# Kernel optimization log

Hardware: AMD Instinct MI355X
Metric: run time of the kernel (lower is better)

Reference implementation:

```python
import jax, jax.numpy as jnp
import numpy as np
import math

G = 512        # graphs in batch
N_PER = 256    # nodes per graph (regular batching)
H = 128        # hidden_size == rnn_hidden_size
DEG = 8        # avg degree
RATIO = 0.8    # TopKPooling ratio
N = G * N_PER
E = N * DEG
N_HIDDEN = 3   # n_hidden_layers


def setup_inputs() -> dict:
    key = jax.random.key(0)
    ks = jax.random.split(key, 20)
    x = jax.random.normal(ks[0], (N, H), jnp.float32)
    m = N_PER * DEG
    src_l = jax.random.randint(ks[1], (G, m), 0, N_PER)
    dst_l = jax.random.randint(ks[2], (G, m), 0, N_PER)
    off = (jnp.arange(G, dtype=jnp.int32) * N_PER)[:, None]
    edge_index = jnp.stack([(src_l + off).reshape(-1), (dst_l + off).reshape(-1)]).astype(jnp.int32)
    s = 1.0 / math.sqrt(H)
    def w(k, shape):
        return jax.random.normal(k, shape, jnp.float32) * s
    return {
        'x': x, 'edge_index': edge_index,
        'W0': w(ks[3], (H, H)), 'b0': jnp.zeros((H,), jnp.float32), 'p0': w(ks[4], (H,)),
        'W1': w(ks[5], (H, H)), 'b1': jnp.zeros((H,), jnp.float32), 'p1': w(ks[6], (H,)),
        'W2': w(ks[7], (H, H)), 'b2': jnp.zeros((H,), jnp.float32), 'p2': w(ks[8], (H,)),
        'Wg': w(ks[9], (H, 1)), 'bg': jnp.zeros((1,), jnp.float32),
    }


def _gcn(x, src, dst, w_e, W, b, n_nodes):
    # GCNConv with self loops: out = D^-1/2 (A+I) D^-1/2 (x W) + b, masked edges have w_e=0
    h = x @ W
    deg = jax.ops.segment_sum(w_e, dst, num_segments=n_nodes) + 1.0  # +1 self loop
    dinv = jax.lax.rsqrt(deg)
    norm = w_e * dinv[src] * dinv[dst]
    agg = jax.ops.segment_sum(h[src] * norm[:, None], dst, num_segments=n_nodes)
    agg = agg + h * (dinv * dinv)[:, None]   # self-loop term
    return agg + b


def _topk(x, src, dst, w_e, p, n_per):
    # TopKPooling: score = x.p/||p||, keep top ceil(ratio*n) per graph, scale by tanh(score)
    k = math.ceil(RATIO * n_per)
    score = (x @ p) / jnp.linalg.norm(p)
    _, idx = jax.lax.top_k(score.reshape(G, n_per), k)           # [G,k] local idx
    perm = (idx + (jnp.arange(G, dtype=idx.dtype) * n_per)[:, None]).reshape(-1)
    x_new = x[perm] * jnp.tanh(score[perm])[:, None]
    nmap = jnp.full((G * n_per,), -1, jnp.int32).at[perm].set(jnp.arange(G * k, dtype=jnp.int32))
    ms, md = nmap[src], nmap[dst]
    valid = (ms >= 0) & (md >= 0)
    src2 = jnp.where(valid, ms, 0)
    dst2 = jnp.where(valid, md, 0)
    return x_new, src2, dst2, w_e * valid.astype(w_e.dtype), k


def _attpool(x, n_per, Wg, bg):
    # GlobalAttention: softmax(gate) over nodes of each graph, weighted sum
    gate = (x @ Wg + bg).reshape(G, n_per)
    a = jax.nn.softmax(gate, axis=1)
    return jnp.einsum('gn,gnh->gh', a, x.reshape(G, n_per, H))


def reference(x, edge_index, W0, b0, p0, W1, b1, p1, W2, b2, p2, Wg, bg):
    src, dst = edge_index[0], edge_index[1]
    w_e = jnp.ones((E,), jnp.float32)
    n_per = N_PER
    h = jax.nn.relu(_gcn(x, src, dst, w_e, W0, b0, G * n_per))
    h, src, dst, w_e, n_per = _topk(h, src, dst, w_e, p0, n_per)
    out = _attpool(h, n_per, Wg, bg)
    for (W, b, p) in ((W1, b1, p1), (W2, b2, p2)):  # n_hidden_layers - 1 = 2
        h = jax.nn.relu(_gcn(h, src, dst, w_e, W, b, G * n_per))
        h, src, dst, w_e, n_per = _topk(h, src, dst, w_e, p, n_per)
        out = out + _attpool(h, n_per, Wg, bg)
    return out
```

## Files before the change

### kernel.cpp

```cpp
#include <hip/hip_runtime.h>
#include <math.h>

#define GCOUNT 512
#define HDIM 128
#define EPG 2048
#define E_TOTAL (GCOUNT * EPG)
#define DEADE 0xFFFFFFFFu

typedef __attribute__((ext_vector_type(8))) short short8;
typedef __attribute__((ext_vector_type(4))) float f32x4;

__device__ inline unsigned short f2bf(float f) {
  unsigned int u = __float_as_uint(f);
  return (unsigned short)((u + 0x7FFFu + ((u >> 16) & 1u)) >> 16);
}
__device__ inline float bf2f(unsigned short s) {
  return __uint_as_float(((unsigned int)s) << 16);
}

__global__ __launch_bounds__(256) void k_wsplit(const float* __restrict__ W,
                                                unsigned short* __restrict__ out) {
  int t = blockIdx.x * 256 + threadIdx.x;
  int lane = t & 63;
  int ct = (t >> 6) & 7;
  int kc = t >> 9;
  int kbase = kc * 32 + (lane >> 4) * 8;
  int col = ct * 16 + (lane & 15);
#pragma unroll
  for (int j = 0; j < 8; j++) {
    float w = W[(size_t)(kbase + j) * HDIM + col];
    unsigned short h0 = f2bf(w);  float g0 = bf2f(h0);
    float r1 = w - g0;
    unsigned short h1 = f2bf(r1); float g1 = bf2f(h1);
    unsigned short h2 = f2bf(r1 - g1);
    int base = (kc * 8 + ct) * 512 + lane * 8 + j;
    out[base]         = h0;
    out[base + 16384] = h1;
    out[base + 32768] = h2;
  }
}

__global__ __launch_bounds__(1024, 1) void k_net(
    const float* __restrict__ xIn, const int* __restrict__ ei0,
    const unsigned short* __restrict__ Ws0,
    const unsigned short* __restrict__ Ws1,
    const unsigned short* __restrict__ Ws2,
    const float* __restrict__ b0, const float* __restrict__ p0,
    const float* __restrict__ b1, const float* __restrict__ p1,
    const float* __restrict__ b2, const float* __restrict__ p2,
    const float* __restrict__ Wg, const float* __restrict__ bgp,
    float* __restrict__ outp) {

  __shared__ __align__(16) float h_s[256 * 132];
  __shared__ unsigned int es[EPG];
  __shared__ unsigned short ss[EPG];
  __shared__ __align__(16) int deg[256];
  __shared__ int cnt[256];
  __shared__ int ofs[256];
  __shared__ int rp[260];
  __shared__ float dinv_s[256];
  __shared__ float rawsc_s[256];
  __shared__ float hd[256];
  __shared__ float sc[256];
  __shared__ int   idx[256];
  __shared__ float tn[256];
  __shared__ float accout[128];
  __shared__ float part[512];
  __shared__ float red[8];
  __shared__ float snorm_s;

  int g = blockIdx.x, t = threadIdx.x;
  int lane = t & 63, wv = t >> 6;
  int eb = g * EPG;
  float bgv = bgp[0];

  if (t < 256) deg[t] = 0;
  if (t < 128) accout[t] = 0.f;
  __syncthreads();
  {
    const float4* xg = (const float4*)(xIn + (size_t)g * 256 * HDIM);
    for (int i = t; i < 8192; i += 1024) {
      int r = i >> 5, q = i & 31;
      *(float4*)&h_s[r * 132 + (q << 2)] = xg[i];
    }
  }
#pragma unroll
  for (int q = 0; q < 2; q++) {
    int e = t + q * 1024;
    int s_ = ei0[eb + e] - g * 256;
    int d_ = ei0[E_TOTAL + eb + e] - g * 256;
    es[e] = (unsigned)s_ | ((unsigned)d_ << 16);
    atomicAdd(&deg[d_], 1);
  }
  __syncthreads();

  int n = 256;
#pragma unroll 1
  for (int layer = 0; layer < 3; layer++) {
    const unsigned short* Ws = (layer == 0) ? Ws0 : (layer == 1 ? Ws1 : Ws2);
    const float* bias = (layer == 0) ? b0 : (layer == 1 ? b1 : b2);
    const float* p    = (layer == 0) ? p0 : (layer == 1 ? p1 : p2);
    int k = (layer == 0) ? 205 : (layer == 1 ? 164 : 132);
    int T = (n + 15) >> 4;

    if (wv < T) {
      int rbase = wv * 16;
      int arow = lane & 15, kgrp = (lane >> 4) * 8;
      f32x4 acc[8];
#pragma unroll
      for (int ct = 0; ct < 8; ct++) acc[ct] = (f32x4){0.f, 0.f, 0.f, 0.f};
#pragma unroll
      for (int kc = 0; kc < 4; kc++) {
        short8 fa0, fa1, fa2;
        {
          const float* ap = &h_s[(rbase + arow) * 132 + kc * 32 + kgrp];
          float4 x0 = *(const float4*)ap;
          float4 x1 = *(const float4*)(ap + 4);
          float v[8] = {x0.x, x0.y, x0.z, x0.w, x1.x, x1.y, x1.z, x1.w};
#pragma unroll
          for (int j = 0; j < 8; j++) {
            float a = v[j];
            unsigned short q0 = f2bf(a);  float g0 = bf2f(q0);
            float r1 = a - g0;
            unsigned short q1 = f2bf(r1); float g1 = bf2f(q1);
            unsigned short q2 = f2bf(r1 - g1);
            fa0[j] = (short)q0; fa1[j] = (short)q1; fa2[j] = (short)q2;
          }
        }
#pragma unroll
        for (int ct = 0; ct < 8; ct++) {
          const unsigned short* wb = Ws + (kc * 8 + ct) * 512 + lane * 8;
          short8 w0 = *(const short8*)wb;
          short8 w1 = *(const short8*)(wb + 16384);
          short8 w2 = *(const short8*)(wb + 32768);
          acc[ct] = __builtin_amdgcn_mfma_f32_16x16x32_bf16(fa0, w0, acc[ct], 0, 0, 0);
          acc[ct] = __builtin_amdgcn_mfma_f32_16x16x32_bf16(fa0, w1, acc[ct], 0, 0, 0);
          acc[ct] = __builtin_amdgcn_mfma_f32_16x16x32_bf16(fa1, w0, acc[ct], 0, 0, 0);
          acc[ct] = __builtin_amdgcn_mfma_f32_16x16x32_bf16(fa1, w1, acc[ct], 0, 0, 0);
          acc[ct] = __builtin_amdgcn_mfma_f32_16x16x32_bf16(fa0, w2, acc[ct], 0, 0, 0);
          acc[ct] = __builtin_amdgcn_mfma_f32_16x16x32_bf16(fa2, w0, acc[ct], 0, 0, 0);
        }
      }
      int crow = (lane >> 4) * 4, ccol = lane & 15;
#pragma unroll
      for (int ct = 0; ct < 8; ct++)
#pragma unroll
        for (int reg = 0; reg < 4; reg++)
          h_s[(rbase + crow + reg) * 132 + ct * 16 + ccol] = acc[ct][reg];
    }
    __syncthreads();

    if (t < 256) dinv_s[t] = rsqrtf((float)deg[t] + 1.0f);
    if (wv == 0) {
      int4 c4 = *(const int4*)&deg[lane << 2];
      int s4 = c4.x + c4.y + c4.z + c4.w;
      int run = s4;
#pragma unroll
      for (int o = 1; o < 64; o <<= 1) {
        int v = __shfl_up(run, o);
        if (lane >= o) run += v;
      }
      int base = run - s4;
      int v1 = base + c4.x, v2 = v1 + c4.y, v3 = v2 + c4.z;
      int li = lane << 2;
      rp[li] = base; rp[li + 1] = v1; rp[li + 2] = v2; rp[li + 3] = v3;
      ofs[li] = base; ofs[li + 1] = v1; ofs[li + 2] = v2; ofs[li + 3] = v3;
      if (lane == 63) rp[256] = run;
    }
    if (wv == 1) {
      float q = p[lane] * p[lane] + p[lane + 64] * p[lane + 64];
#pragma unroll
      for (int o = 32; o > 0; o >>= 1) q += __shfl_xor(q, o);
      if (lane == 0) snorm_s = sqrtf(q);
    }
    if (t >= 128 && t < 512) {
      int i = t - 128;
      part[i] = (i < 128) ? bias[i] : (i < 256 ? p[i - 128] : Wg[i - 256]);
    }
    __syncthreads();

    if (t < 256) { cnt[t] = -1; deg[t] = 0; }
    for (int e = t; e < EPG; e += 1024) {
      unsigned u = es[e];
      if (u != DEADE) {
        int pos = atomicAdd(&ofs[u >> 16], 1);
        ss[pos] = (unsigned short)(u & 0xFFFFu);
      }
    }
    __syncthreads();

    {
      int dstT = t >> 2;
      int cq = (t & 3) << 3;
      bool dok = dstT < n;
      int begT = 0, endT = 0;
      float dvT = 0.f;
      if (dok) { begT = rp[dstT]; endT = rp[dstT + 1]; dvT = dinv_s[dstT]; }
      float sp = 0.f, sg = 0.f;
#pragma unroll 1
      for (int grp = 0; grp < 4; grp++) {
        int c0 = (grp << 5) + cq;
        float4 r0 = make_float4(0.f, 0.f, 0.f, 0.f);
        float4 r1 = make_float4(0.f, 0.f, 0.f, 0.f);
        if (dok) {
          float4 u0 = make_float4(0.f, 0.f, 0.f, 0.f);
          float4 u1 = make_float4(0.f, 0.f, 0.f, 0.f);
          int j = begT;
          for (; j + 2 <= endT; j += 2) {
            int sa = ss[j], sb = ss[j + 1];
            float wa = dinv_s[sa], wb2 = dinv_s[sb];
            const float* ha = &h_s[sa * 132 + c0];
            const float* hbp = &h_s[sb * 132 + c0];
            float4 xa0 = *(const float4*)ha;
            float4 xa1 = *(const float4*)(ha + 4);
            float4 xb0 = *(const float4*)hbp;
            float4 xb1 = *(const float4*)(hbp + 4);
            u0.x = fmaf(wa, xa0.x, u0.x); u0.y = fmaf(wa, xa0.y, u0.y);
            u0.z = fmaf(wa, xa0.z, u0.z); u0.w = fmaf(wa, xa0.w, u0.w);
            u1.x = fmaf(wa, xa1.x, u1.x); u1.y = fmaf(wa, xa1.y, u1.y);
            u1.z = fmaf(wa, xa1.z, u1.z); u1.w = fmaf(wa, xa1.w, u1.w);
            u0.x = fmaf(wb2, xb0.x, u0.x); u0.y = fmaf(wb2, xb0.y, u0.y);
            u0.z = fmaf(wb2, xb0.z, u0.z); u0.w = fmaf(wb2, xb0.w, u0.w);
            u1.x = fmaf(wb2, xb1.x, u1.x); u1.y = fmaf(wb2, xb1.y, u1.y);
            u1.z = fmaf(wb2, xb1.z, u1.z); u1.w = fmaf(wb2, xb1.w, u1.w);
          }
          if (j < endT) {
            int sa = ss[j];
            float wa = dinv_s[sa];
            const float* ha = &h_s[sa * 132 + c0];
            float4 xa0 = *(const float4*)ha;
            float4 xa1 = *(const float4*)(ha + 4);
            u0.x = fmaf(wa, xa0.x, u0.x); u0.y = fmaf(wa, xa0.y, u0.y);
            u0.z = fmaf(wa, xa0.z, u0.z); u0.w = fmaf(wa, xa0.w, u0.w);
            u1.x = fmaf(wa, xa1.x, u1.x); u1.y = fmaf(wa, xa1.y, u1.y);
            u1.z = fmaf(wa, xa1.z, u1.z); u1.w = fmaf(wa, xa1.w, u1.w);
          }
          const float* hdp = &h_s[dstT * 132 + c0];
          float4 s0 = *(const float4*)hdp;
          float4 s1 = *(const float4*)(hdp + 4);
          float4 bb0 = *(const float4*)&part[c0];
          float4 bb1 = *(const float4*)&part[c0 + 4];
          r0.x = fmaxf(fmaf(dvT, fmaf(s0.x, dvT, u0.x), bb0.x), 0.f);
          r0.y = fmaxf(fmaf(dvT, fmaf(s0.y, dvT, u0.y), bb0.y), 0.f);
          r0.z = fmaxf(fmaf(dvT, fmaf(s0.z, dvT, u0.z), bb0.z), 0.f);
          r0.w = fmaxf(fmaf(dvT, fmaf(s0.w, dvT, u0.w), bb0.w), 0.f);
          r1.x = fmaxf(fmaf(dvT, fmaf(s1.x, dvT, u1.x), bb1.x), 0.f);
          r1.y = fmaxf(fmaf(dvT, fmaf(s1.y, dvT, u1.y), bb1.y), 0.f);
          r1.z = fmaxf(fmaf(dvT, fmaf(s1.z, dvT, u1.z), bb1.z), 0.f);
          r1.w = fmaxf(fmaf(dvT, fmaf(s1.w, dvT, u1.w), bb1.w), 0.f);
          float4 pp0 = *(const float4*)&part[128 + c0];
          float4 pp1 = *(const float4*)&part[128 + c0 + 4];
          float4 gg0 = *(const float4*)&part[256 + c0];
          float4 gg1 = *(const float4*)&part[256 + c0 + 4];
          sp += r0.x * pp0.x + r0.y * pp0.y + r0.z * pp0.z + r0.w * pp0.w
              + r1.x * pp1.x + r1.y * pp1.y + r1.z * pp1.z + r1.w * pp1.w;
          sg += r0.x * gg0.x + r0.y * gg0.y + r0.z * gg0.z + r0.w * gg0.w
              + r1.x * gg1.x + r1.y * gg1.y + r1.z * gg1.z + r1.w * gg1.w;
        }
        __syncthreads();
        if (dok) {
          *(float4*)&h_s[dstT * 132 + c0] = r0;
          *(float4*)&h_s[dstT * 132 + c0 + 4] = r1;
        }
      }
      __syncthreads();
      sp += __shfl_xor(sp, 1); sp += __shfl_xor(sp, 2);
      sg += __shfl_xor(sg, 1); sg += __shfl_xor(sg, 2);
      if (dok && (t & 3) == 0) { rawsc_s[dstT] = sp; hd[dstT] = sg; }
    }
    __syncthreads();

    float key = -INFINITY;
    int id = t & 255;
    if (t < n) key = rawsc_s[t];
    for (int size = 2; size <= 256; size <<= 1) {
      for (int stride = size >> 1; stride > 0; stride >>= 1) {
        if (stride > 32) {
          if (t < 256) { sc[t] = key; idx[t] = id; }
          __syncthreads();
          float pk = 0.f; int pi = 0;
          if (t < 256) { pk = sc[t ^ stride]; pi = idx[t ^ stride]; }
          __syncthreads();
          if (t < 256) {
            bool want = ((t & size) == 0);
            bool lowr = ((t & stride) == 0);
            bool mineFirst = (key > pk) || (key == pk && id < pi);
            if (mineFirst != (want == lowr)) { key = pk; id = pi; }
          }
        } else {
          if (t < 256) {
            float pk = __shfl_xor(key, stride);
            int pi = __shfl_xor(id, stride);
            bool want = ((t & size) == 0);
            bool lowr = ((t & stride) == 0);
            bool mineFirst = (key > pk) || (key == pk && id < pi);
            if (mineFirst != (want == lowr)) { key = pk; id = pi; }
          }
        }
      }
    }
    if (t < 256) idx[t] = id;
    __syncthreads();

    float gate = -INFINITY;
    if (t < k) {
      float tnv = tanhf(key / snorm_s);
      tn[t] = tnv;
      cnt[id] = t;
      gate = fmaf(hd[id], tnv, bgv);
    }
    if (wv < 4) {
      float m = gate;
#pragma unroll
      for (int o = 32; o > 0; o >>= 1) m = fmaxf(m, __shfl_xor(m, o));
      if (lane == 0) red[wv] = m;
    }
    __syncthreads();

    float ex = 0.f;
    if (wv < 4) {
      float m = fmaxf(fmaxf(red[0], red[1]), fmaxf(red[2], red[3]));
      ex = (t < k) ? __expf(gate - m) : 0.f;
      float s = ex;
#pragma unroll
      for (int o = 32; o > 0; o >>= 1) s += __shfl_xor(s, o);
      if (lane == 0) red[4 + wv] = s;
    } else if (wv >= 8 && layer < 2) {
      int tt = t - 512;
#pragma unroll
      for (int q = 0; q < 4; q++) {
        int e = tt + q * 512;
        unsigned u = es[e];
        unsigned o = DEADE;
        if (u != DEADE) {
          int ns = cnt[u & 0xFFFFu], nd = cnt[u >> 16];
          if (ns >= 0 && nd >= 0) o = (unsigned)ns | ((unsigned)nd << 16);
        }
        es[e] = o;
        if (o != DEADE) atomicAdd(&deg[o >> 16], 1);
      }
    }
    __syncthreads();

    if (t < 256) {
      float inv = 1.f / (red[4] + red[5] + red[6] + red[7]);
      float a = (t < k) ? ex * inv : 0.f;
      sc[t] = (layer == 2) ? a * tn[t] : a;
    }
    __syncthreads();

    if (layer < 2) {
      {
        int rT = t >> 2;
        int cq4 = (t & 3) << 3;
        bool rok = rT < k;
        int src = 0;
        float tr = 0.f;
        if (rok) { src = idx[rT]; tr = tn[rT]; }
#pragma unroll 1
        for (int grp = 0; grp < 4; grp++) {
          int c0 = (grp << 5) + cq4;
          float4 v0 = make_float4(0.f, 0.f, 0.f, 0.f);
          float4 v1 = make_float4(0.f, 0.f, 0.f, 0.f);
          if (rok) {
            const float* hp = &h_s[src * 132 + c0];
            v0 = *(const float4*)hp;
            v1 = *(const float4*)(hp + 4);
            v0.x *= tr; v0.y *= tr; v0.z *= tr; v0.w *= tr;
            v1.x *= tr; v1.y *= tr; v1.z *= tr; v1.w *= tr;
          }
          __syncthreads();
          if (rok) {
            *(float4*)&h_s[rT * 132 + c0] = v0;
            *(float4*)&h_s[rT * 132 + c0 + 4] = v1;
          }
        }
      }
      __syncthreads();
      if (t < 512) {
        int grp = t >> 7, c2 = t & 127;
        float pp = 0.f;
        for (int r = grp; r < k; r += 4) pp = fmaf(sc[r], h_s[r * 132 + c2], pp);
        part[t] = pp;
      }
      __syncthreads();
      if (t < 128) accout[t] += part[t] + part[128 + t] + part[256 + t] + part[384 + t];
      __syncthreads();
    } else {
      if (t < 512) {
        int grp = t >> 7, c2 = t & 127;
        float pp = 0.f;
        for (int r = grp; r < k; r += 4) pp = fmaf(sc[r], h_s[idx[r] * 132 + c2], pp);
        part[t] = pp;
      }
      __syncthreads();
      if (t < 128)
        outp[(size_t)g * HDIM + t] =
            accout[t] + part[t] + part[128 + t] + part[256 + t] + part[384 + t];
    }
    n = k;
  }
}

extern "C" void kernel_launch(void* const* d_in, const int* in_sizes, int n_in,
                              void* d_out, int out_size, void* d_ws, size_t ws_size,
                              hipStream_t stream) {
  const float* x  = (const float*)d_in[0];
  const int*   ei = (const int*)d_in[1];
  const float* W0 = (const float*)d_in[2];
  const float* b0 = (const float*)d_in[3];
  const float* p0 = (const float*)d_in[4];
  const float* W1 = (const float*)d_in[5];
  const float* b1 = (const float*)d_in[6];
  const float* p1 = (const float*)d_in[7];
  const float* W2 = (const float*)d_in[8];
  const float* b2 = (const float*)d_in[9];
  const float* p2 = (const float*)d_in[10];
  const float* Wg = (const float*)d_in[11];
  const float* bg = (const float*)d_in[12];
  float* out = (float*)d_out;

  unsigned char* ws = (unsigned char*)d_ws;
  unsigned short* Wsp0 = (unsigned short*)(ws);
  unsigned short* Wsp1 = (unsigned short*)(ws + 98304ull);
  unsigned short* Wsp2 = (unsigned short*)(ws + 196608ull);

  k_wsplit<<<8, 256, 0, stream>>>(W0, Wsp0);
  k_wsplit<<<8, 256, 0, stream>>>(W1, Wsp1);
  k_wsplit<<<8, 256, 0, stream>>>(W2, Wsp2);
  k_net<<<GCOUNT, 1024, 0, stream>>>(x, ei, Wsp0, Wsp1, Wsp2,
                                     b0, p0, b1, p1, b2, p2, Wg, bg, out);
}
```

Measured before the change: 233.7 us.

## Use 2-term bf16 split GEMM, halve aggregation passes, double-buffer bitonic sort

The weight and activation splitting drops from three bf16 terms to two, cutting MFMAs per tile from 6 to 4 and removing the third weight load. The GCN aggregation and top-k gather now process two 64-column halves per thread instead of four 32-column groups, which halves the edge-list walks and the barriers. The bitonic sort's cross-wave stages ping-pong between two shared buffers, so each stage needs one barrier instead of two. The reduced split lowers GEMM precision, which could change top-k selections on near-ties.

```diff
diff --git a/kernel.cpp b/kernel.cpp
--- a/kernel.cpp
+++ b/kernel.cpp
@@ -16,6 +16,26 @@
 }
 __device__ inline float bf2f(unsigned short s) {
   return __uint_as_float(((unsigned int)s) << 16);
+}
+__device__ inline float4 z4() { return make_float4(0.f, 0.f, 0.f, 0.f); }
+__device__ inline float4 ld4(const float* p) { return *(const float4*)p; }
+__device__ inline void fma4(float4& u, float w, float4 x) {
+  u.x = fmaf(w, x.x, u.x); u.y = fmaf(w, x.y, u.y);
+  u.z = fmaf(w, x.z, u.z); u.w = fmaf(w, x.w, u.w);
+}
+__device__ inline float4 fin4(float4 u, float4 s, float4 b, float dv) {
+  float4 r;
+  r.x = fmaxf(fmaf(dv, fmaf(s.x, dv, u.x), b.x), 0.f);
+  r.y = fmaxf(fmaf(dv, fmaf(s.y, dv, u.y), b.y), 0.f);
+  r.z = fmaxf(fmaf(dv, fmaf(s.z, dv, u.z), b.z), 0.f);
+  r.w = fmaxf(fmaf(dv, fmaf(s.w, dv, u.w), b.w), 0.f);
+  return r;
+}
+__device__ inline float dot4(float4 a, float4 b) {
+  return a.x * b.x + a.y * b.y + a.z * b.z + a.w * b.w;
+}
+__device__ inline float4 scale4(float4 v, float s) {
+  v.x *= s; v.y *= s; v.z *= s; v.w *= s; return v;
 }
 
 __global__ __launch_bounds__(256) void k_wsplit(const float* __restrict__ W,
@@ -30,13 +50,10 @@
   for (int j = 0; j < 8; j++) {
     float w = W[(size_t)(kbase + j) * HDIM + col];
     unsigned short h0 = f2bf(w);  float g0 = bf2f(h0);
-    float r1 = w - g0;
-    unsigned short h1 = f2bf(r1); float g1 = bf2f(h1);
-    unsigned short h2 = f2bf(r1 - g1);
+    unsigned short h1 = f2bf(w - g0);
     int base = (kc * 8 + ct) * 512 + lane * 8 + j;
     out[base]         = h0;
     out[base + 16384] = h1;
-    out[base + 32768] = h2;
   }
 }
 
@@ -111,20 +128,18 @@
       for (int ct = 0; ct < 8; ct++) acc[ct] = (f32x4){0.f, 0.f, 0.f, 0.f};
 #pragma unroll
       for (int kc = 0; kc < 4; kc++) {
-        short8 fa0, fa1, fa2;
+        short8 fa0, fa1;
         {
           const float* ap = &h_s[(rbase + arow) * 132 + kc * 32 + kgrp];
-          float4 x0 = *(const float4*)ap;
-          float4 x1 = *(const float4*)(ap + 4);
+          float4 x0 = ld4(ap);
+          float4 x1 = ld4(ap + 4);
           float v[8] = {x0.x, x0.y, x0.z, x0.w, x1.x, x1.y, x1.z, x1.w};
 #pragma unroll
           for (int j = 0; j < 8; j++) {
             float a = v[j];
-            unsigned short q0 = f2bf(a);  float g0 = bf2f(q0);
-            float r1 = a - g0;
-            unsigned short q1 = f2bf(r1); float g1 = bf2f(q1);
-            unsigned short q2 = f2bf(r1 - g1);
-            fa0[j] = (short)q0; fa1[j] = (short)q1; fa2[j] = (short)q2;
+            unsigned short q0 = f2bf(a);
+            unsigned short q1 = f2bf(a - bf2f(q0));
+            fa0[j] = (short)q0; fa1[j] = (short)q1;
           }
         }
 #pragma unroll
@@ -132,13 +147,10 @@
           const unsigned short* wb = Ws + (kc * 8 + ct) * 512 + lane * 8;
           short8 w0 = *(const short8*)wb;
           short8 w1 = *(const short8*)(wb + 16384);
-          short8 w2 = *(const short8*)(wb + 32768);
           acc[ct] = __builtin_amdgcn_mfma_f32_16x16x32_bf16(fa0, w0, acc[ct], 0, 0, 0);
           acc[ct] = __builtin_amdgcn_mfma_f32_16x16x32_bf16(fa0, w1, acc[ct], 0, 0, 0);
           acc[ct] = __builtin_amdgcn_mfma_f32_16x16x32_bf16(fa1, w0, acc[ct], 0, 0, 0);
           acc[ct] = __builtin_amdgcn_mfma_f32_16x16x32_bf16(fa1, w1, acc[ct], 0, 0, 0);
-          acc[ct] = __builtin_amdgcn_mfma_f32_16x16x32_bf16(fa0, w2, acc[ct], 0, 0, 0);
-          acc[ct] = __builtin_amdgcn_mfma_f32_16x16x32_bf16(fa2, w0, acc[ct], 0, 0, 0);
         }
       }
       int crow = (lane >> 4) * 4, ccol = lane & 15;
@@ -193,77 +205,60 @@
       int dstT = t >> 2;
       int cq = (t & 3) << 3;
       bool dok = dstT < n;
-      int begT = 0, endT = 0;
-      float dvT = 0.f;
+      int begT = 0, endT = 0; float dvT = 0.f;
       if (dok) { begT = rp[dstT]; endT = rp[dstT + 1]; dvT = dinv_s[dstT]; }
       float sp = 0.f, sg = 0.f;
-#pragma unroll 1
-      for (int grp = 0; grp < 4; grp++) {
-        int c0 = (grp << 5) + cq;
-        float4 r0 = make_float4(0.f, 0.f, 0.f, 0.f);
-        float4 r1 = make_float4(0.f, 0.f, 0.f, 0.f);
-        if (dok) {
-          float4 u0 = make_float4(0.f, 0.f, 0.f, 0.f);
-          float4 u1 = make_float4(0.f, 0.f, 0.f, 0.f);
-          int j = begT;
-          for (; j + 2 <= endT; j += 2) {
-            int sa = ss[j], sb = ss[j + 1];
-            float wa = dinv_s[sa], wb2 = dinv_s[sb];
-            const float* ha = &h_s[sa * 132 + c0];
-            const float* hbp = &h_s[sb * 132 + c0];
-            float4 xa0 = *(const float4*)ha;
-            float4 xa1 = *(const float4*)(ha + 4);
-            float4 xb0 = *(const float4*)hbp;
-            float4 xb1 = *(const float4*)(hbp + 4);
-            u0.x = fmaf(wa, xa0.x, u0.x); u0.y = fmaf(wa, xa0.y, u0.y);
-            u0.z = fmaf(wa, xa0.z, u0.z); u0.w = fmaf(wa, xa0.w, u0.w);
-            u1.x = fmaf(wa, xa1.x, u1.x); u1.y = fmaf(wa, xa1.y, u1.y);
-            u1.z = fmaf(wa, xa1.z, u1.z); u1.w = fmaf(wa, xa1.w, u1.w);
-            u0.x = fmaf(wb2, xb0.x, u0.x); u0.y = fmaf(wb2, xb0.y, u0.y);
-            u0.z = fmaf(wb2, xb0.z, u0.z); u0.w = fmaf(wb2, xb0.w, u0.w);
-            u1.x = fmaf(wb2, xb1.x, u1.x); u1.y = fmaf(wb2, xb1.y, u1.y);
-            u1.z = fmaf(wb2, xb1.z, u1.z); u1.w = fmaf(wb2, xb1.w, u1.w);
-          }
-          if (j < endT) {
-            int sa = ss[j];
-            float wa = dinv_s[sa];
-            const float* ha = &h_s[sa * 132 + c0];
-            float4 xa0 = *(const float4*)ha;
-            float4 xa1 = *(const float4*)(ha + 4);
-            u0.x = fmaf(wa, xa0.x, u0.x); u0.y = fmaf(wa, xa0.y, u0.y);
-            u0.z = fmaf(wa, xa0.z, u0.z); u0.w = fmaf(wa, xa0.w, u0.w);
-            u1.x = fmaf(wa, xa1.x, u1.x); u1.y = fmaf(wa, xa1.y, u1.y);
-            u1.z = fmaf(wa, xa1.z, u1.z); u1.w = fmaf(wa, xa1.w, u1.w);
-          }
-          const float* hdp = &h_s[dstT * 132 + c0];
-          float4 s0 = *(const float4*)hdp;
-          float4 s1 = *(const float4*)(hdp + 4);
-          float4 bb0 = *(const float4*)&part[c0];
-          float4 bb1 = *(const float4*)&part[c0 + 4];
-          r0.x = fmaxf(fmaf(dvT, fmaf(s0.x, dvT, u0.x), bb0.x), 0.f);
-          r0.y = fmaxf(fmaf(dvT, fmaf(s0.y, dvT, u0.y), bb0.y), 0.f);
-          r0.z = fmaxf(fmaf(dvT, fmaf(s0.z, dvT, u0.z), bb0.z), 0.f);
-          r0.w = fmaxf(fmaf(dvT, fmaf(s0.w, dvT, u0.w), bb0.w), 0.f);
-          r1.x = fmaxf(fmaf(dvT, fmaf(s1.x, dvT, u1.x), bb1.x), 0.f);
-          r1.y = fmaxf(fmaf(dvT, fmaf(s1.y, dvT, u1.y), bb1.y), 0.f);
-          r1.z = fmaxf(fmaf(dvT, fmaf(s1.z, dvT, u1.z), bb1.z), 0.f);
-          r1.w = fmaxf(fmaf(dvT, fmaf(s1.w, dvT, u1.w), bb1.w), 0.f);
-          float4 pp0 = *(const float4*)&part[128 + c0];
-          float4 pp1 = *(const float4*)&part[128 + c0 + 4];
-          float4 gg0 = *(const float4*)&part[256 + c0];
-          float4 gg1 = *(const float4*)&part[256 + c0 + 4];
-          sp += r0.x * pp0.x + r0.y * pp0.y + r0.z * pp0.z + r0.w * pp0.w
-              + r1.x * pp1.x + r1.y * pp1.y + r1.z * pp1.z + r1.w * pp1.w;
-          sg += r0.x * gg0.x + r0.y * gg0.y + r0.z * gg0.z + r0.w * gg0.w
-              + r1.x * gg1.x + r1.y * gg1.y + r1.z * gg1.z + r1.w * gg1.w;
-        }
-        __syncthreads();
-        if (dok) {
-          *(float4*)&h_s[dstT * 132 + c0] = r0;
-          *(float4*)&h_s[dstT * 132 + c0 + 4] = r1;
-        }
-      }
-      __syncthreads();
+      float4 rA0, rA1, rB0, rB1;
+      if (dok) {
+        float4 uA0 = z4(), uA1 = z4(), uB0 = z4(), uB1 = z4();
+        for (int j = begT; j < endT; ++j) {
+          int sa = ss[j];
+          float wa = dinv_s[sa];
+          const float* ha = &h_s[sa * 132 + cq];
+          fma4(uA0, wa, ld4(ha));      fma4(uA1, wa, ld4(ha + 4));
+          fma4(uB0, wa, ld4(ha + 32)); fma4(uB1, wa, ld4(ha + 36));
+        }
+        const float* hdp = &h_s[dstT * 132 + cq];
+        rA0 = fin4(uA0, ld4(hdp),      ld4(&part[cq]),      dvT);
+        rA1 = fin4(uA1, ld4(hdp + 4),  ld4(&part[cq + 4]),  dvT);
+        rB0 = fin4(uB0, ld4(hdp + 32), ld4(&part[32 + cq]), dvT);
+        rB1 = fin4(uB1, ld4(hdp + 36), ld4(&part[32 + cq + 4]), dvT);
+        sp += dot4(rA0, ld4(&part[128 + cq])) + dot4(rA1, ld4(&part[128 + cq + 4]))
+            + dot4(rB0, ld4(&part[160 + cq])) + dot4(rB1, ld4(&part[160 + cq + 4]));
+        sg += dot4(rA0, ld4(&part[256 + cq])) + dot4(rA1, ld4(&part[256 + cq + 4]))
+            + dot4(rB0, ld4(&part[288 + cq])) + dot4(rB1, ld4(&part[288 + cq + 4]));
+      }
+      __syncthreads();
+      if (dok) {
+        float* hw = &h_s[dstT * 132 + cq];
+        *(float4*)hw = rA0; *(float4*)(hw + 4) = rA1;
+        *(float4*)(hw + 32) = rB0; *(float4*)(hw + 36) = rB1;
+      }
+      if (dok) {
+        float4 uA0 = z4(), uA1 = z4(), uB0 = z4(), uB1 = z4();
+        for (int j = begT; j < endT; ++j) {
+          int sa = ss[j];
+          float wa = dinv_s[sa];
+          const float* ha = &h_s[sa * 132 + 64 + cq];
+          fma4(uA0, wa, ld4(ha));      fma4(uA1, wa, ld4(ha + 4));
+          fma4(uB0, wa, ld4(ha + 32)); fma4(uB1, wa, ld4(ha + 36));
+        }
+        const float* hdp = &h_s[dstT * 132 + 64 + cq];
+        rA0 = fin4(uA0, ld4(hdp),      ld4(&part[64 + cq]),  dvT);
+        rA1 = fin4(uA1, ld4(hdp + 4),  ld4(&part[64 + cq + 4]), dvT);
+        rB0 = fin4(uB0, ld4(hdp + 32), ld4(&part[96 + cq]),  dvT);
+        rB1 = fin4(uB1, ld4(hdp + 36), ld4(&part[96 + cq + 4]), dvT);
+        sp += dot4(rA0, ld4(&part[192 + cq])) + dot4(rA1, ld4(&part[192 + cq + 4]))
+            + dot4(rB0, ld4(&part[224 + cq])) + dot4(rB1, ld4(&part[224 + cq + 4]));
+        sg += dot4(rA0, ld4(&part[320 + cq])) + dot4(rA1, ld4(&part[320 + cq + 4]))
+            + dot4(rB0, ld4(&part[352 + cq])) + dot4(rB1, ld4(&part[352 + cq + 4]));
+      }
+      __syncthreads();
+      if (dok) {
+        float* hw = &h_s[dstT * 132 + 64 + cq];
+        *(float4*)hw = rA0; *(float4*)(hw + 4) = rA1;
+        *(float4*)(hw + 32) = rB0; *(float4*)(hw + 36) = rB1;
+      }
       sp += __shfl_xor(sp, 1); sp += __shfl_xor(sp, 2);
       sg += __shfl_xor(sg, 1); sg += __shfl_xor(sg, 2);
       if (dok && (t & 3) == 0) { rawsc_s[dstT] = sp; hd[dstT] = sg; }
@@ -273,32 +268,38 @@
     float key = -INFINITY;
     int id = t & 255;
     if (t < n) key = rawsc_s[t];
-    for (int size = 2; size <= 256; size <<= 1) {
-      for (int stride = size >> 1; stride > 0; stride >>= 1) {
-        if (stride > 32) {
-          if (t < 256) { sc[t] = key; idx[t] = id; }
-          __syncthreads();
-          float pk = 0.f; int pi = 0;
-          if (t < 256) { pk = sc[t ^ stride]; pi = idx[t ^ stride]; }
-          __syncthreads();
-          if (t < 256) {
-            bool want = ((t & size) == 0);
-            bool lowr = ((t & stride) == 0);
-            bool mineFirst = (key > pk) || (key == pk && id < pi);
-            if (mineFirst != (want == lowr)) { key = pk; id = pi; }
+    {
+      int pp = 0;
+      for (int size = 2; size <= 256; size <<= 1) {
+        for (int stride = size >> 1; stride > 0; stride >>= 1) {
+          if (stride > 32) {
+            float* sb = pp ? (float*)part : sc;
+            int* ib = pp ? ofs : idx;
+            if (t < 256) { sb[t] = key; ib[t] = id; }
+            __syncthreads();
+            if (t < 256) {
+              float pk = sb[t ^ stride];
+              int pi = ib[t ^ stride];
+              bool want = ((t & size) == 0);
+              bool lowr = ((t & stride) == 0);
+              bool mineFirst = (key > pk) || (key == pk && id < pi);
+              if (mineFirst != (want == lowr)) { key = pk; id = pi; }
+            }
+            pp ^= 1;
+          } else {
+            if (t < 256) {
+              float pk = __shfl_xor(key, stride);
+              int pi = __shfl_xor(id, stride);
+              bool want = ((t & size) == 0);
+              bool lowr = ((t & stride) == 0);
+              bool mineFirst = (key > pk) || (key == pk && id < pi);
+              if (mineFirst != (want == lowr)) { key = pk; id = pi; }
+            }
           }
-        } else {
-          if (t < 256) {
-            float pk = __shfl_xor(key, stride);
-            int pi = __shfl_xor(id, stride);
-            bool want = ((t & size) == 0);
-            bool lowr = ((t & stride) == 0);
-            bool mineFirst = (key > pk) || (key == pk && id < pi);
-            if (mineFirst != (want == lowr)) { key = pk; id = pi; }
-          }
-        }
-      }
-    }
+        }
+      }
+    }
+    __syncthreads();
     if (t < 256) idx[t] = id;
     __syncthreads();
 
@@ -354,34 +355,38 @@
         int rT = t >> 2;
         int cq4 = (t & 3) << 3;
         bool rok = rT < k;
-        int src = 0;
-        float tr = 0.f;
+        int src = 0; float tr = 0.f;
         if (rok) { src = idx[rT]; tr = tn[rT]; }
-#pragma unroll 1
-        for (int grp = 0; grp < 4; grp++) {
-          int c0 = (grp << 5) + cq4;
-          float4 v0 = make_float4(0.f, 0.f, 0.f, 0.f);
-          float4 v1 = make_float4(0.f, 0.f, 0.f, 0.f);
-          if (rok) {
-            const float* hp = &h_s[src * 132 + c0];
-            v0 = *(const float4*)hp;
-            v1 = *(const float4*)(hp + 4);
-            v0.x *= tr; v0.y *= tr; v0.z *= tr; v0.w *= tr;
-            v1.x *= tr; v1.y *= tr; v1.z *= tr; v1.w *= tr;
-          }
-          __syncthreads();
-          if (rok) {
-            *(float4*)&h_s[rT * 132 + c0] = v0;
-            *(float4*)&h_s[rT * 132 + c0 + 4] = v1;
-          }
+        float4 vA0, vA1, vB0, vB1;
+        if (rok) {
+          const float* hp = &h_s[src * 132 + cq4];
+          vA0 = scale4(ld4(hp), tr);      vA1 = scale4(ld4(hp + 4), tr);
+          vB0 = scale4(ld4(hp + 32), tr); vB1 = scale4(ld4(hp + 36), tr);
+        }
+        __syncthreads();
+        if (rok) {
+          float* hw = &h_s[rT * 132 + cq4];
+          *(float4*)hw = vA0; *(float4*)(hw + 4) = vA1;
+          *(float4*)(hw + 32) = vB0; *(float4*)(hw + 36) = vB1;
+        }
+        if (rok) {
+          const float* hp = &h_s[src * 132 + 64 + cq4];
+          vA0 = scale4(ld4(hp), tr);      vA1 = scale4(ld4(hp + 4), tr);
+          vB0 = scale4(ld4(hp + 32), tr); vB1 = scale4(ld4(hp + 36), tr);
+        }
+        __syncthreads();
+        if (rok) {
+          float* hw = &h_s[rT * 132 + 64 + cq4];
+          *(float4*)hw = vA0; *(float4*)(hw + 4) = vA1;
+          *(float4*)(hw + 32) = vB0; *(float4*)(hw + 36) = vB1;
         }
       }
       __syncthreads();
       if (t < 512) {
         int grp = t >> 7, c2 = t & 127;
-        float pp = 0.f;
-        for (int r = grp; r < k; r += 4) pp = fmaf(sc[r], h_s[r * 132 + c2], pp);
-        part[t] = pp;
+        float pp2 = 0.f;
+        for (int r = grp; r < k; r += 4) pp2 = fmaf(sc[r], h_s[r * 132 + c2], pp2);
+        part[t] = pp2;
       }
       __syncthreads();
       if (t < 128) accout[t] += part[t] + part[128 + t] + part[256 + t] + part[384 + t];
@@ -389,9 +394,9 @@
     } else {
       if (t < 512) {
         int grp = t >> 7, c2 = t & 127;
-        float pp = 0.f;
-        for (int r = grp; r < k; r += 4) pp = fmaf(sc[r], h_s[idx[r] * 132 + c2], pp);
-        part[t] = pp;
+        float pp2 = 0.f;
+        for (int r = grp; r < k; r += 4) pp2 = fmaf(sc[r], h_s[idx[r] * 132 + c2], pp2);
+        part[t] = pp2;
       }
       __syncthreads();
       if (t < 128)
```

After: 201.3 us (median of 3 runs). 13.9% less time.
